# Kernel tuning notes

Hardware: AMD Instinct MI355X
Metric: run time of the kernel (lower is better)

Reference implementation:

```python
import jax, jax.numpy as jnp
import numpy as np

E, H, LQ, LC, B = 1024, 16, 1024, 512, 4
HD = E // H
FF = 4 * E
EPS = 1e-6


def _rope(x):
    # x: [B, H, L, D]; interleaved rotary embedding (lucidrains-style)
    D, L = x.shape[-1], x.shape[-2]
    inv_freq = 1.0 / (10000.0 ** (jnp.arange(0, D, 2, dtype=jnp.float32) / D))
    ang = jnp.arange(L, dtype=jnp.float32)[:, None] * inv_freq[None, :]  # [L, D/2]
    cos, sin = jnp.cos(ang), jnp.sin(ang)
    x1, x2 = x[..., 0::2], x[..., 1::2]
    r1 = x1 * cos - x2 * sin
    r2 = x1 * sin + x2 * cos
    return jnp.stack([r1, r2], axis=-1).reshape(x.shape)


def _ln(x, w, b):
    mu = jnp.mean(x, -1, keepdims=True)
    var = jnp.mean(jnp.square(x - mu), -1, keepdims=True)
    return (x - mu) * jax.lax.rsqrt(var + EPS) * w + b


def _rope_attn(x, ctx, qw, qb, kw, kb, vw, vb, pw, pb, mask):
    Bn, L, Em = x.shape
    Lc = ctx.shape[1]
    q = (x @ qw.T + qb).reshape(Bn, L, H, HD).transpose(0, 2, 1, 3)
    k = (ctx @ kw.T + kb).reshape(Bn, Lc, H, HD).transpose(0, 2, 1, 3)
    v = (ctx @ vw.T + vb).reshape(Bn, Lc, H, HD).transpose(0, 2, 1, 3)
    q, k = _rope(q), _rope(k)
    s = jnp.einsum('bhic,bhjc->bhij', q, k) / np.sqrt(HD).astype(np.float32)
    if mask is not None:
        s = jnp.where(mask[None, None], -jnp.inf, s)
    p = jax.nn.softmax(s, axis=-1)
    o = jnp.einsum('bhij,bhjc->bhic', p, v)
    o = o.transpose(0, 2, 1, 3).reshape(Bn, L, Em)
    return o @ pw.T + pb


def setup_inputs() -> dict:
    key = jax.random.key(0)
    ks = iter(jax.random.split(key, 40))
    s = 0.02
    d = {}
    d['x'] = jax.random.normal(next(ks), (B, LQ, E), jnp.float32)
    d['context'] = jax.random.normal(next(ks), (B, LC, E), jnp.float32)
    d['attn_mask'] = jnp.triu(jnp.ones((LQ, LQ), bool), k=1)  # True = masked (causal)
    for g in ('g_msa', 'g_ca', 'g_mlp'):
        d[g] = jax.random.normal(next(ks), (1, 1, E), jnp.float32) * s
    for n in ('n1', 'n2', 'n3'):
        d[n + '_w'] = jnp.ones((E,), jnp.float32)
        d[n + '_b'] = jnp.zeros((E,), jnp.float32)
    for p in ('sa', 'ca'):
        for m in ('q', 'k', 'v', 'p'):
            d[f'{p}_{m}w'] = jax.random.normal(next(ks), (E, E), jnp.float32) * s
            d[f'{p}_{m}b'] = jnp.zeros((E,), jnp.float32)
    d['fc1_w'] = jax.random.normal(next(ks), (FF, E), jnp.float32) * s
    d['fc1_b'] = jnp.zeros((FF,), jnp.float32)
    d['fc2_w'] = jax.random.normal(next(ks), (E, FF), jnp.float32) * s
    d['fc2_b'] = jnp.zeros((E,), jnp.float32)
    return d


def reference(x, context, attn_mask,
              g_msa, g_ca, g_mlp,
              n1_w, n1_b, n2_w, n2_b, n3_w, n3_b,
              sa_qw, sa_qb, sa_kw, sa_kb, sa_vw, sa_vb, sa_pw, sa_pb,
              ca_qw, ca_qb, ca_kw, ca_kb, ca_vw, ca_vb, ca_pw, ca_pb,
              fc1_w, fc1_b, fc2_w, fc2_b):
    # self-attention (causal RoPE) with zero-init learned gate
    x = x + g_msa * _rope_attn(_ln(x, n1_w, n1_b), _ln(x, n1_w, n1_b),
                               sa_qw, sa_qb, sa_kw, sa_kb, sa_vw, sa_vb,
                               sa_pw, sa_pb, attn_mask)
    # cross-attention (RoPE on both streams, no mask)
    h = _ln(x, n2_w, n2_b)
    x = x + g_ca * _rope_attn(h, context,
                              ca_qw, ca_qb, ca_kw, ca_kb, ca_vw, ca_vb,
                              ca_pw, ca_pb, None)
    # gated MLP with tanh-approx GELU
    h = _ln(x, n3_w, n3_b)
    h = jax.nn.gelu(h @ fc1_w.T + fc1_b, approximate=True) @ fc2_w.T + fc2_b
    x = x + g_mlp * h
    return x
```

## Files before the change

### kernel.cpp

```cpp
#include <hip/hip_runtime.h>
#include <math.h>

#if !__has_builtin(__builtin_amdgcn_cvt_pk_fp8_f32)
#include <hip/hip_fp8.h>
#endif

typedef __attribute__((ext_vector_type(8))) short short8;
typedef __attribute__((ext_vector_type(4))) float f32x4;
typedef __attribute__((ext_vector_type(16))) float f32x16;
typedef unsigned char u8;
typedef unsigned short u16;
typedef unsigned int u32;
typedef __attribute__((ext_vector_type(2))) u32 u32x2;
typedef __attribute__((ext_vector_type(4))) u32 u32x4;
typedef __attribute__((ext_vector_type(8))) int i32x8;
typedef unsigned long long u64;

static constexpr int E = 1024, H = 16, LQ = 1024, LC = 512, Bn = 4, FF = 4096;
static constexpr int NTOK = Bn * LQ;
static constexpr int NCTX = Bn * LC;

#define QSCALE 0.1803368801111244f
#define DEFER_THR 11.5f

static constexpr size_t OFF_TCOS   = 0;
static constexpr size_t OFF_TSIN   = OFF_TCOS + (size_t)LQ*32*4;
static constexpr size_t OFF_BSAQKV = OFF_TSIN + (size_t)LQ*32*4;
static constexpr size_t OFF_BCAKV  = OFF_BSAQKV + 16384;
static constexpr size_t OFF_WSAQKV = OFF_BCAKV + 16384;
static constexpr size_t OFF_WSAP   = OFF_WSAQKV + (size_t)3072*1024*2;
static constexpr size_t OFF_WCAQ   = OFF_WSAP   + (size_t)1024*1024*2;
static constexpr size_t OFF_WCAKV  = OFF_WCAQ   + (size_t)1024*1024*2;
static constexpr size_t OFF_WCAP   = OFF_WCAKV  + (size_t)2048*1024*2;
static constexpr size_t OFF_WFC1   = OFF_WCAP   + (size_t)1024*1024*2;
static constexpr size_t OFF_WFC2   = OFF_WFC1   + (size_t)4096*1024*2;
static constexpr size_t OFF_CTXB   = OFF_WFC2   + (size_t)1024*4096*2;
static constexpr size_t OFF_H      = OFF_CTXB   + (size_t)2048*1024*2;
static constexpr size_t OFF_QKV    = OFF_H      + (size_t)4096*1024*2;
static constexpr size_t OFF_CAQ    = OFF_QKV;
static constexpr size_t OFF_CAKV   = OFF_QKV + (size_t)4096*1024*2;
static constexpr size_t OFF_QR     = OFF_QKV + (size_t)4096*3072*2;
static constexpr size_t OFF_KR     = OFF_QR  + (size_t)4096*1024*2;
static constexpr size_t OFF_VT     = OFF_KR  + (size_t)4096*1024*2;
static constexpr size_t OFF_AO     = OFF_VT  + (size_t)4096*1024*2;
static constexpr size_t OFF_U      = OFF_QKV;
static constexpr size_t WS_NEED    = OFF_AO + (size_t)4096*1024*2;

static __device__ __forceinline__ float bf2f(u16 u) {
  union { u32 i; float f; } un; un.i = ((u32)u) << 16; return un.f;
}
static __device__ __forceinline__ u16 f2bf(float f) {
  union { float f; u32 u; } un; un.f = f;
  u32 u = un.u;
  return (u16)((u + 0x7FFFu + ((u >> 16) & 1u)) >> 16);
}
static __device__ __forceinline__ u64 pack4(u16 a, u16 b, u16 c, u16 d) {
  return (u64)a | ((u64)b << 16) | ((u64)c << 32) | ((u64)d << 48);
}
static __device__ __forceinline__ f32x4 mfma16(short8 a, short8 b, f32x4 c) {
  return __builtin_amdgcn_mfma_f32_16x16x32_bf16(a, b, c, 0, 0, 0);
}
static __device__ __forceinline__ f32x16 mfma32(short8 a, short8 b, f32x16 c) {
  return __builtin_amdgcn_mfma_f32_32x32x16_bf16(a, b, c, 0, 0, 0);
}
static __device__ __forceinline__ void gload_lds16(void* lds, const void* g) {
  __builtin_amdgcn_global_load_lds(
      (const __attribute__((address_space(1))) void*)g,
      (__attribute__((address_space(3))) void*)lds, 16, 0, 0);
}
static __device__ __forceinline__ float gelu_tanh(float x) {
  float z2 = 1.5957691216057308f * (x + 0.044715f * x * x * x);
  float e = __expf(z2);
  float r = __builtin_amdgcn_rcpf(e + 1.0f);
  return x - x * r;
}
static __device__ __forceinline__ u32 cvtpk_bf16(float lo, float hi) {
  u32 r;
  asm("v_cvt_pk_bf16_f32 %0, %1, %2" : "=v"(r) : "v"(lo), "v"(hi));
  return r;
}
static __device__ __forceinline__ u32 pack_fp8x4(float a, float b, float c, float d) {
#if __has_builtin(__builtin_amdgcn_cvt_pk_fp8_f32)
  u32 r = (u32)__builtin_amdgcn_cvt_pk_fp8_f32(a, b, 0, false);
  r = (u32)__builtin_amdgcn_cvt_pk_fp8_f32(c, d, (int)r, true);
  return r;
#else
  __hip_fp8_e4m3 qa(a), qb(b), qc(c), qd(d);
  return (u32)qa.__x | ((u32)qb.__x << 8) | ((u32)qc.__x << 16) | ((u32)qd.__x << 24);
#endif
}
static __device__ __forceinline__ u8 fp8b(float f) {
#if __has_builtin(__builtin_amdgcn_cvt_pk_fp8_f32)
  return (u8)((u32)__builtin_amdgcn_cvt_pk_fp8_f32(f, f, 0, false) & 0xFFu);
#else
  __hip_fp8_e4m3 t(f); return t.__x;
#endif
}

__global__ __launch_bounds__(256) void build_tab(float* __restrict__ ct, float* __restrict__ st) {
  int idx = blockIdx.x * 256 + threadIdx.x;
  int pos = idx >> 5, i = idx & 31;
  float inv = powf(10000.f, -(float)i * (1.f / 32.f));
  float a = (float)pos * inv;
  ct[idx] = cosf(a);
  st[idx] = sinf(a);
}

struct Cvt11 { const float* s[11]; };
__global__ __launch_bounds__(256) void cvt_all(Cvt11 a, u16* __restrict__ dst) {
  u32 gid = blockIdx.x * 256 + threadIdx.x;
  u32 s, off;
  if (gid < 2097152u)      { s = gid >> 18;                        off = gid & 262143u; }
  else if (gid < 4194304u) { return; }
  else                     { s = 10;                               off = gid - 4194304u; }
  float4 v = *(const float4*)(a.s[s] + (size_t)off * 4);
  *(u64*)(dst + (size_t)gid * 4) = pack4(f2bf(v.x), f2bf(v.y), f2bf(v.z), f2bf(v.w));
}

__global__ __launch_bounds__(256) void cvt_fp8(const float* __restrict__ s0, const float* __restrict__ s1,
                                               u8* __restrict__ d0, u8* __restrict__ d1) {
  u32 gid = blockIdx.x * 256 + threadIdx.x;
  const float* s; u8* d; u32 off;
  if (gid < 1048576u) { s = s0; d = d0; off = gid; }
  else                { s = s1; d = d1; off = gid - 1048576u; }
  float4 v = *(const float4*)(s + (size_t)off * 4);
  *(u32*)(d + (size_t)off * 4) =
      pack_fp8x4(v.x * 256.f, v.y * 256.f, v.z * 256.f, v.w * 256.f);
}

struct Cp5 { const float* s[5]; };
__global__ __launch_bounds__(256) void copy5(Cp5 a, float* __restrict__ dst) {
  int gid = blockIdx.x * 256 + threadIdx.x;
  int s = gid >> 10, off = gid & 1023;
  int doff = (s < 3) ? s * 1024 : 4096 + (s - 3) * 1024;
  dst[doff + off] = a.s[s][off];
}

__global__ __launch_bounds__(256) void ln_bf16(const float* __restrict__ x, const float* __restrict__ w,
                                               const float* __restrict__ b, u16* __restrict__ out) {
  __shared__ float red[4];
  int row = blockIdx.x, tid = threadIdx.x;
  const float* xr = x + (size_t)row * 1024;
  float4 v = ((const float4*)xr)[tid];
  float s = v.x + v.y + v.z + v.w;
#pragma unroll
  for (int off = 32; off; off >>= 1) s += __shfl_xor(s, off);
  if ((tid & 63) == 0) red[tid >> 6] = s;
  __syncthreads();
  float mean = (red[0] + red[1] + red[2] + red[3]) * (1.f / 1024.f);
  float dx = v.x - mean, dy = v.y - mean, dz = v.z - mean, dw = v.w - mean;
  float sq = dx * dx + dy * dy + dz * dz + dw * dw;
#pragma unroll
  for (int off = 32; off; off >>= 1) sq += __shfl_xor(sq, off);
  __syncthreads();
  if ((tid & 63) == 0) red[tid >> 6] = sq;
  __syncthreads();
  float var = (red[0] + red[1] + red[2] + red[3]) * (1.f / 1024.f);
  float rstd = rsqrtf(var + 1e-6f);
  float4 wv = ((const float4*)w)[tid];
  float4 bv = ((const float4*)b)[tid];
  u64 o = pack4(f2bf(dx * rstd * wv.x + bv.x), f2bf(dy * rstd * wv.y + bv.y),
                f2bf(dz * rstd * wv.z + bv.z), f2bf(dw * rstd * wv.w + bv.w));
  *(u64*)(out + (size_t)row * 1024 + tid * 4) = o;
}

__global__ __launch_bounds__(256) void ln_fp8(const float* __restrict__ x, const float* __restrict__ w,
                                              const float* __restrict__ b, u8* __restrict__ out) {
  __shared__ float red[4];
  int row = blockIdx.x, tid = threadIdx.x;
  const float* xr = x + (size_t)row * 1024;
  float4 v = ((const float4*)xr)[tid];
  float s = v.x + v.y + v.z + v.w;
#pragma unroll
  for (int off = 32; off; off >>= 1) s += __shfl_xor(s, off);
  if ((tid & 63) == 0) red[tid >> 6] = s;
  __syncthreads();
  float mean = (red[0] + red[1] + red[2] + red[3]) * (1.f / 1024.f);
  float dx = v.x - mean, dy = v.y - mean, dz = v.z - mean, dw = v.w - mean;
  float sq = dx * dx + dy * dy + dz * dz + dw * dw;
#pragma unroll
  for (int off = 32; off; off >>= 1) sq += __shfl_xor(sq, off);
  __syncthreads();
  if ((tid & 63) == 0) red[tid >> 6] = sq;
  __syncthreads();
  float var = (red[0] + red[1] + red[2] + red[3]) * (1.f / 1024.f);
  float rstd = rsqrtf(var + 1e-6f);
  float4 wv = ((const float4*)w)[tid];
  float4 bv = ((const float4*)b)[tid];
  u32 pk = pack_fp8x4((dx * rstd * wv.x + bv.x) * 16.f, (dy * rstd * wv.y + bv.y) * 16.f,
                      (dz * rstd * wv.z + bv.z) * 16.f, (dw * rstd * wv.w + bv.w) * 16.f);
  *(u32*)(out + (size_t)row * 1024 + tid * 4) = pk;
}

struct RopeJob { const u16* src; u16* dst; int ld, col0, Lper, T, mode; float scale; };
struct Rope3 { RopeJob j[3]; };
__global__ __launch_bounds__(128) void rope3(Rope3 a, const float* __restrict__ cosT,
                                             const float* __restrict__ sinT) {
  RopeJob jb = a.j[blockIdx.y];
  int t = blockIdx.x;
  if (t >= jb.T) return;
  int b = t / jb.Lper, l = t - b * jb.Lper;
  int tid = threadIdx.x;
  int e0 = tid * 8;
  int h = e0 >> 6, d0 = e0 & 63;
  short8 vv = *(const short8*)(jb.src + (size_t)t * jb.ld + jb.col0 + e0);
  if (jb.mode == 0) {
    short8 ov;
#pragma unroll
    for (int j = 0; j < 4; ++j) {
      float x1 = bf2f((u16)vv[2 * j]);
      float x2 = bf2f((u16)vv[2 * j + 1]);
      int i = (d0 >> 1) + j;
      float c = cosT[l * 32 + i], s = sinT[l * 32 + i];
      ov[2 * j]     = (short)f2bf((x1 * c - x2 * s) * jb.scale);
      ov[2 * j + 1] = (short)f2bf((x1 * s + x2 * c) * jb.scale);
    }
    *(short8*)(jb.dst + (((size_t)b * H + h) * jb.Lper + l) * 64 + d0) = ov;
  } else {
#pragma unroll
    for (int m = 0; m < 8; ++m)
      jb.dst[(((size_t)b * H + h) * 64 + d0 + m) * jb.Lper + l] = (u16)vv[m];
  }
}

enum { EPI_BF16 = 0, EPI_GELU = 1, EPI_RESID = 2 };

template <int EPI>
__global__ __launch_bounds__(512, 4) void gemm2(const u16* __restrict__ A, const u16* __restrict__ W,
                                                const float* __restrict__ bias, u16* outb, float* outf,
                                                const float* res, const float* __restrict__ gate,
                                                int M, int N, int K) {
  __shared__ u16 As[2][128 * 64];
  __shared__ u16 Bs[2][128 * 64];

  int nwg = gridDim.x * gridDim.y;
  int bid = blockIdx.y * gridDim.x + blockIdx.x;
  int cpx = nwg >> 3;
  int swz = (bid & 7) * cpx + (bid >> 3);
  int bx = swz % gridDim.x;
  int by = swz / gridDim.x;
  int row0 = by * 128, col0 = bx * 128;

  int tid = threadIdx.x;
  int lane = tid & 63, wid = tid >> 6;
  int wr = wid >> 2, wc = wid & 3;
  int lr = lane & 15, lg = lane >> 4;

  size_t a_off0, a_off1, b_off0, b_off1;
  int l_off0 = tid * 8, l_off1 = (512 + tid) * 8;
  {
    int q = tid, r = q >> 3, p = q & 7, sp = p ^ (r & 7);
    a_off0 = (size_t)(row0 + r) * K + sp * 8;
    b_off0 = (size_t)(col0 + r) * K + sp * 8;
    q = 512 + tid; r = q >> 3; p = q & 7; sp = p ^ (r & 7);
    a_off1 = (size_t)(row0 + r) * K + sp * 8;
    b_off1 = (size_t)(col0 + r) * K + sp * 8;
  }

  f32x4 acc[4][2] = {};

  const int nkt = K >> 6;
  {
    gload_lds16(&As[0][l_off0], A + a_off0);
    gload_lds16(&Bs[0][l_off0], W + b_off0);
    gload_lds16(&As[0][l_off1], A + a_off1);
    gload_lds16(&Bs[0][l_off1], W + b_off1);
  }
  __syncthreads();

  for (int kt = 0; kt < nkt; ++kt) {
    int cur = kt & 1;
    if (kt + 1 < nkt) {
      int k0 = (kt + 1) << 6;
      gload_lds16(&As[cur ^ 1][l_off0], A + a_off0 + k0);
      gload_lds16(&Bs[cur ^ 1][l_off0], W + b_off0 + k0);
      gload_lds16(&As[cur ^ 1][l_off1], A + a_off1 + k0);
      gload_lds16(&Bs[cur ^ 1][l_off1], W + b_off1 + k0);
    }
#pragma unroll
    for (int kk = 0; kk < 2; ++kk) {
      short8 af[4], bfr[2];
#pragma unroll
      for (int m = 0; m < 4; ++m) {
        int r = wr * 64 + m * 16 + lr;
        int sc = (kk * 4 + lg) ^ (r & 7);
        af[m] = *(const short8*)(&As[cur][r * 64 + sc * 8]);
      }
#pragma unroll
      for (int n = 0; n < 2; ++n) {
        int r = wc * 32 + n * 16 + lr;
        int sc = (kk * 4 + lg) ^ (r & 7);
        bfr[n] = *(const short8*)(&Bs[cur][r * 64 + sc * 8]);
      }
#pragma unroll
      for (int m = 0; m < 4; ++m)
#pragma unroll
        for (int n = 0; n < 2; ++n)
          acc[m][n] = mfma16(af[m], bfr[n], acc[m][n]);
    }
    __syncthreads();
  }

  if (EPI == EPI_BF16 || EPI == EPI_GELU) {
    u16* Ct = &As[0][0];
#pragma unroll
    for (int n = 0; n < 2; ++n) {
      int c = wc * 32 + n * 16 + lr;
      float bv = bias[col0 + c];
#pragma unroll
      for (int m = 0; m < 4; ++m) {
#pragma unroll
        for (int i = 0; i < 4; ++i) {
          int r = wr * 64 + m * 16 + lg * 4 + i;
          float v = acc[m][n][i] + bv;
          Ct[r * 128 + c] = f2bf(EPI == EPI_GELU ? gelu_tanh(v) : v);
        }
      }
    }
    __syncthreads();
#pragma unroll
    for (int j = 0; j < 4; ++j) {
      u32 q = (u32)tid + j * 512;
      u32 r = q >> 4, ck = q & 15;
      short8 v = *(const short8*)(Ct + r * 128 + ck * 8);
      *(short8*)(outb + (size_t)(row0 + r) * N + col0 + ck * 8) = v;
    }
  } else {
#pragma unroll
    for (int n = 0; n < 2; ++n) {
      int cg = col0 + wc * 32 + n * 16 + lr;
      float bv = bias[cg];
#pragma unroll
      for (int m = 0; m < 4; ++m) {
#pragma unroll
        for (int i = 0; i < 4; ++i) {
          int rg = row0 + wr * 64 + m * 16 + lg * 4 + i;
          float v = acc[m][n][i] + bv;
          float r = res[(size_t)rg * N + cg];
          outf[(size_t)rg * N + cg] = r + gate[cg] * v;
        }
      }
    }
  }
}

enum { E8_GELU = 0, E8_RESID = 1 };

template <int EPI>
__global__ __launch_bounds__(256, 2) void gemm8(const u8* __restrict__ A, const u8* __restrict__ W,
                                                const float* __restrict__ bias, u8* outb, float* outf,
                                                const float* res, const float* __restrict__ gate,
                                                int M, int N, int K) {
  __shared__ u8 As[2][128 * 128];
  __shared__ u8 Bs[2][128 * 128];

  int nwg = gridDim.x * gridDim.y;
  int bid = blockIdx.y * gridDim.x + blockIdx.x;
  int cpx = nwg >> 3;
  int swz = (bid & 7) * cpx + (bid >> 3);
  int bx = swz % gridDim.x, by = swz / gridDim.x;
  int row0 = by * 128, col0 = bx * 128;

  int tid = threadIdx.x;
  int lane = tid & 63, wid = tid >> 6;
  int wr = wid >> 1, wc = wid & 1;
  int lr = lane & 15, lg = lane >> 4;

  u32 aoff[4], boff[4];
  int ldso[4];
#pragma unroll
  for (int j = 0; j < 4; ++j) {
    int q = tid + j * 256;
    int r = q >> 3, p = q & 7, sp = p ^ (r & 7);
    aoff[j] = (u32)(row0 + r) * (u32)K + sp * 16;
    boff[j] = (u32)(col0 + r) * (u32)K + sp * 16;
    ldso[j] = q * 16;
  }

  f32x4 acc[4][4] = {};
  const int nkt = K >> 7;

  auto rdfrag = [&](const u8* base, int r, i32x8& f) {
    const u8* rp = base + r * 128;
    int ck = lg * 2;
    u32x4 lo = *(const u32x4*)(rp + ((ck) ^ (r & 7)) * 16);
    u32x4 hh = *(const u32x4*)(rp + ((ck + 1) ^ (r & 7)) * 16);
    i32x8 v;
    v[0] = (int)lo[0]; v[1] = (int)lo[1]; v[2] = (int)lo[2]; v[3] = (int)lo[3];
    v[4] = (int)hh[0]; v[5] = (int)hh[1]; v[6] = (int)hh[2]; v[7] = (int)hh[3];
    f = v;
  };

#pragma unroll
  for (int j = 0; j < 4; ++j) {
    gload_lds16(&As[0][ldso[j]], A + aoff[j]);
    gload_lds16(&Bs[0][ldso[j]], W + boff[j]);
  }
  __syncthreads();

  for (int kt = 0; kt < nkt; ++kt) {
    int cur = kt & 1;
    if (kt + 1 < nkt) {
      int k0 = (kt + 1) << 7;
#pragma unroll
      for (int j = 0; j < 4; ++j) {
        gload_lds16(&As[cur ^ 1][ldso[j]], A + aoff[j] + k0);
        gload_lds16(&Bs[cur ^ 1][ldso[j]], W + boff[j] + k0);
      }
    }
    i32x8 a[4], b[4];
#pragma unroll
    for (int m = 0; m < 4; ++m) rdfrag(&As[cur][0], wr * 64 + m * 16 + lr, a[m]);
#pragma unroll
    for (int n = 0; n < 4; ++n) rdfrag(&Bs[cur][0], wc * 64 + n * 16 + lr, b[n]);
    __builtin_amdgcn_s_setprio(1);
#pragma unroll
    for (int m = 0; m < 4; ++m)
#pragma unroll
      for (int n = 0; n < 4; ++n)
        acc[m][n] = __builtin_amdgcn_mfma_scale_f32_16x16x128_f8f6f4(
            a[m], b[n], acc[m][n], 0, 0, 0, 0x7F7F7F7F, 0, 0x7F7F7F7F);
    __builtin_amdgcn_s_setprio(0);
    __syncthreads();
  }

  constexpr float SCL = 1.f / 4096.f;
  if (EPI == E8_GELU) {
    u8* Ct = &As[0][0];
#pragma unroll
    for (int n = 0; n < 4; ++n) {
      int cl = wc * 64 + n * 16 + lr;
      float bv = bias[col0 + cl];
#pragma unroll
      for (int m = 0; m < 4; ++m) {
#pragma unroll
        for (int i = 0; i < 4; ++i) {
          int rl = wr * 64 + m * 16 + lg * 4 + i;
          float v = acc[m][n][i] * SCL + bv;
          Ct[rl * 128 + cl] = fp8b(gelu_tanh(v) * 16.f);
        }
      }
    }
    __syncthreads();
#pragma unroll
    for (int j = 0; j < 4; ++j) {
      int q = tid + j * 256;
      int r = q >> 3, ck = q & 7;
      *(u32x4*)(outb + (size_t)(row0 + r) * N + col0 + ck * 16) =
          *(const u32x4*)(Ct + r * 128 + ck * 16);
    }
  } else {
#pragma unroll
    for (int n = 0; n < 4; ++n) {
      int cg = col0 + wc * 64 + n * 16 + lr;
      float bv = bias[cg], gv = gate[cg];
#pragma unroll
      for (int m = 0; m < 4; ++m) {
#pragma unroll
        for (int i = 0; i < 4; ++i) {
          int rg = row0 + wr * 64 + m * 16 + lg * 4 + i;
          float v = acc[m][n][i] * SCL + bv;
          float r = res[(size_t)rg * N + cg];
          outf[(size_t)rg * N + cg] = r + gv * v;
        }
      }
    }
  }
}

template <int MASKED, int PRE>
static __device__ __forceinline__ void attn_tile3(short8* kf, const u16* KtNext,
                                                  const u16* Vp0, const u16* Vp1,
                                                  const short8* qf, int kb, int q0, int l31, int hi,
                                                  float& m, float& lsum, f32x16& o0, f32x16& o1) {
  short8 vf0[4], vf1[4];
#pragma unroll
  for (int ks = 0; ks < 4; ++ks) {
    vf0[ks] = *(const short8*)(Vp0 + ks * 16 + hi * 8);
    vf1[ks] = *(const short8*)(Vp1 + ks * 16 + hi * 8);
  }
  f32x16 s0 = {}, s1 = {};
  __builtin_amdgcn_s_setprio(1);
#pragma unroll
  for (int s = 0; s < 4; ++s) {
    s0 = mfma32(kf[s], qf[s], s0);
    s1 = mfma32(kf[4 + s], qf[s], s1);
  }
  __builtin_amdgcn_s_setprio(0);
  if (PRE) {
    const u16* kp0 = KtNext + (size_t)l31 * 64 + hi * 8;
    const u16* kp1 = KtNext + (size_t)(32 + l31) * 64 + hi * 8;
#pragma unroll
    for (int s = 0; s < 4; ++s) {
      kf[s] = *(const short8*)(kp0 + s * 16);
      kf[4 + s] = *(const short8*)(kp1 + s * 16);
    }
  }
  if (MASKED) {
    int qg = q0 + l31;
#pragma unroll
    for (int r = 0; r < 16; ++r) {
      int kk = kb + (r & 3) + 8 * (r >> 2) + 4 * hi;
      if (kk > qg) s0[r] = -INFINITY;
      if (kk + 32 > qg) s1[r] = -INFINITY;
    }
  }
  float pm = -INFINITY;
#pragma unroll
  for (int r = 0; r < 16; ++r) pm = fmaxf(pm, fmaxf(s0[r], s1[r]));
  pm = fmaxf(pm, __shfl_xor(pm, 32));
  if (!__all(pm <= m + DEFER_THR)) {
    float mn = fmaxf(m, pm);
    float al = exp2f(m - mn);
    m = mn;
    lsum *= al;
#pragma unroll
    for (int r = 0; r < 16; ++r) {
      float alr = __shfl(al, (r & 3) + 8 * (r >> 2) + 4 * hi);
      o0[r] *= alr;
      o1[r] *= alr;
    }
  }
  float ts = 0.f;
#pragma unroll
  for (int r = 0; r < 16; ++r) {
    float p0 = exp2f(s0[r] - m);
    float p1 = exp2f(s1[r] - m);
    s0[r] = p0; s1[r] = p1;
    ts += p0 + p1;
  }
  ts += __shfl_xor(ts, 32);
  lsum += ts;
  auto pack8 = [&](float a0, float a1, float a2, float a3,
                   float a4, float a5, float a6, float a7) -> short8 {
    u32 c0 = cvtpk_bf16(a0, a1), c1 = cvtpk_bf16(a2, a3);
    u32 c2 = cvtpk_bf16(a4, a5), c3 = cvtpk_bf16(a6, a7);
    u32x2 r02 = __builtin_amdgcn_permlane32_swap(c0, c2, false, false);
    u32x2 r13 = __builtin_amdgcn_permlane32_swap(c1, c3, false, false);
    u32x4 w;
    w[0] = r02[0]; w[1] = r13[0]; w[2] = r02[1]; w[3] = r13[1];
    return __builtin_bit_cast(short8, w);
  };
  short8 pa0 = pack8(s0[0], s0[1], s0[2], s0[3], s0[4], s0[5], s0[6], s0[7]);
  short8 pa1 = pack8(s0[8], s0[9], s0[10], s0[11], s0[12], s0[13], s0[14], s0[15]);
  short8 pa2 = pack8(s1[0], s1[1], s1[2], s1[3], s1[4], s1[5], s1[6], s1[7]);
  short8 pa3 = pack8(s1[8], s1[9], s1[10], s1[11], s1[12], s1[13], s1[14], s1[15]);
  short8 pa[4] = {pa0, pa1, pa2, pa3};
  __builtin_amdgcn_s_setprio(1);
#pragma unroll
  for (int ks = 0; ks < 4; ++ks) {
    o0 = mfma32(pa[ks], vf0[ks], o0);
    o1 = mfma32(pa[ks], vf1[ks], o1);
  }
  __builtin_amdgcn_s_setprio(0);
}

template <int CAUSAL>
__global__ __launch_bounds__(256) void flash_attn2(const u16* __restrict__ Q, const u16* __restrict__ K,
                                                   const u16* __restrict__ Vt, u16* __restrict__ O,
                                                   int Lq, int Lk) {
  const int wid = threadIdx.x >> 6, lane = threadIdx.x & 63;
  const int l31 = lane & 31, hi = lane >> 5;
  int wg = blockIdx.x * 4 + wid;
  int bh = wg & 63;
  int qc = wg >> 6;
  if (CAUSAL) qc = (Lq >> 5) - 1 - qc;
  int q0 = qc << 5;

  const u16* Qb = Q + ((size_t)bh * Lq + q0) * 64;
  const u16* Kb = K + (size_t)bh * Lk * 64;
  const u16* Vb = Vt + (size_t)bh * 64 * Lk;

  short8 qf[4];
#pragma unroll
  for (int s = 0; s < 4; ++s) qf[s] = *(const short8*)(Qb + (size_t)l31 * 64 + s * 16 + hi * 8);

  f32x16 o0 = {}, o1 = {};
  float m = -INFINITY, lsum = 0.f;

  const u16* Kt = Kb;
  const u16* Vp0 = Vb + (size_t)l31 * Lk;
  const u16* Vp1 = Vb + (size_t)(32 + l31) * Lk;

  short8 kf[8];
  {
    const u16* kp0 = Kt + (size_t)l31 * 64 + hi * 8;
    const u16* kp1 = Kt + (size_t)(32 + l31) * 64 + hi * 8;
#pragma unroll
    for (int s = 0; s < 4; ++s) {
      kf[s] = *(const short8*)(kp0 + s * 16);
      kf[4 + s] = *(const short8*)(kp1 + s * 16);
    }
  }

  int nt = CAUSAL ? ((q0 >> 6) + 1) : (Lk >> 6);
  for (int t = 0; t < nt - 1; ++t) {
    attn_tile3<0, 1>(kf, Kt + 64 * 64, Vp0, Vp1, qf, t * 64, q0, l31, hi, m, lsum, o0, o1);
    Kt += 64 * 64; Vp0 += 64; Vp1 += 64;
  }
  if (CAUSAL)
    attn_tile3<1, 0>(kf, nullptr, Vp0, Vp1, qf, (nt - 1) * 64, q0, l31, hi, m, lsum, o0, o1);
  else
    attn_tile3<0, 0>(kf, nullptr, Vp0, Vp1, qf, (nt - 1) * 64, q0, l31, hi, m, lsum, o0, o1);

  float myinv = 1.f / lsum;
  int b = bh >> 4, h = bh & 15;
#pragma unroll
  for (int r = 0; r < 16; ++r) {
    int cr = (r & 3) + 8 * (r >> 2) + 4 * hi;
    float li = __shfl(myinv, cr);
    u16* op = O + ((size_t)b * Lq + q0 + cr) * 1024 + h * 64;
    op[l31] = f2bf(o0[r] * li);
    op[32 + l31] = f2bf(o1[r] * li);
  }
}

extern "C" void kernel_launch(void* const* d_in, const int* in_sizes, int n_in,
                              void* d_out, int out_size, void* d_ws, size_t ws_size,
                              hipStream_t stream) {
  (void)in_sizes; (void)n_in; (void)out_size;
  if (ws_size < WS_NEED) return;

  const float* x     = (const float*)d_in[0];
  const float* ctx   = (const float*)d_in[1];
  const float* g_msa = (const float*)d_in[3];
  const float* g_ca  = (const float*)d_in[4];
  const float* g_mlp = (const float*)d_in[5];
  const float* n1w = (const float*)d_in[6],  *n1b = (const float*)d_in[7];
  const float* n2w = (const float*)d_in[8],  *n2b = (const float*)d_in[9];
  const float* n3w = (const float*)d_in[10], *n3b = (const float*)d_in[11];
  const float* sa_qw = (const float*)d_in[12], *sa_kw = (const float*)d_in[14];
  const float* sa_vw = (const float*)d_in[16], *sa_pw = (const float*)d_in[18];
  const float* sa_qb = (const float*)d_in[13], *sa_kb = (const float*)d_in[15];
  const float* sa_vb = (const float*)d_in[17], *sa_pb = (const float*)d_in[19];
  const float* ca_qw = (const float*)d_in[20], *ca_qb = (const float*)d_in[21];
  const float* ca_kw = (const float*)d_in[22], *ca_kb = (const float*)d_in[23];
  const float* ca_vw = (const float*)d_in[24], *ca_vb = (const float*)d_in[25];
  const float* ca_pw = (const float*)d_in[26], *ca_pb = (const float*)d_in[27];
  const float* fc1w = (const float*)d_in[28], *fc1b = (const float*)d_in[29];
  const float* fc2w = (const float*)d_in[30], *fc2b = (const float*)d_in[31];

  char* ws = (char*)d_ws;
  float* out = (float*)d_out;
  float* tcos = (float*)(ws + OFF_TCOS);
  float* tsin = (float*)(ws + OFF_TSIN);
  u16* Hb   = (u16*)(ws + OFF_H);
  u16* QKV  = (u16*)(ws + OFF_QKV);
  u16* QR   = (u16*)(ws + OFF_QR);
  u16* KR   = (u16*)(ws + OFF_KR);
  u16* VT   = (u16*)(ws + OFF_VT);
  u16* AO   = (u16*)(ws + OFF_AO);
  u8*  H8   = (u8*)(ws + OFF_H);
  u8*  U8   = (u8*)(ws + OFF_U);
  u8*  W8FC1 = (u8*)(ws + OFF_QR);
  u8*  W8FC2 = (u8*)(ws + OFF_KR);

  build_tab<<<dim3(128), dim3(256), 0, stream>>>(tcos, tsin);

  Cvt11 ca;
  ca.s[0] = sa_qw; ca.s[1] = sa_kw; ca.s[2] = sa_vw; ca.s[3] = sa_pw;
  ca.s[4] = ca_qw; ca.s[5] = ca_kw; ca.s[6] = ca_vw; ca.s[7] = ca_pw;
  ca.s[8] = fc1w;  ca.s[9] = fc2w;  ca.s[10] = ctx;
  cvt_all<<<dim3(18432), dim3(256), 0, stream>>>(ca, (u16*)(ws + OFF_WSAQKV));
  Cp5 cp;
  cp.s[0] = sa_qb; cp.s[1] = sa_kb; cp.s[2] = sa_vb; cp.s[3] = ca_kb; cp.s[4] = ca_vb;
  copy5<<<dim3(20), dim3(256), 0, stream>>>(cp, (float*)(ws + OFF_BSAQKV));

  ln_bf16<<<dim3(NTOK), dim3(256), 0, stream>>>(x, n1w, n1b, Hb);
  gemm2<EPI_BF16><<<dim3(3072 / 128, NTOK / 128), dim3(512), 0, stream>>>(
      Hb, (u16*)(ws + OFF_WSAQKV), (float*)(ws + OFF_BSAQKV), QKV, nullptr, nullptr, nullptr,
      NTOK, 3072, 1024);
  {
    Rope3 r;
    r.j[0] = {QKV, QR, 3072, 0,    LQ, NTOK, 0, QSCALE};
    r.j[1] = {QKV, KR, 3072, 1024, LQ, NTOK, 0, 1.0f};
    r.j[2] = {QKV, VT, 3072, 2048, LQ, NTOK, 1, 1.0f};
    rope3<<<dim3(NTOK, 3), dim3(128), 0, stream>>>(r, tcos, tsin);
  }
  flash_attn2<1><<<dim3(512), dim3(256), 0, stream>>>(QR, KR, VT, AO, LQ, LQ);
  gemm2<EPI_RESID><<<dim3(1024 / 128, NTOK / 128), dim3(512), 0, stream>>>(
      AO, (u16*)(ws + OFF_WSAP), sa_pb, nullptr, out, x, g_msa, NTOK, 1024, 1024);

  ln_bf16<<<dim3(NTOK), dim3(256), 0, stream>>>(out, n2w, n2b, Hb);
  gemm2<EPI_BF16><<<dim3(1024 / 128, NTOK / 128), dim3(512), 0, stream>>>(
      Hb, (u16*)(ws + OFF_WCAQ), ca_qb, (u16*)(ws + OFF_CAQ), nullptr, nullptr, nullptr,
      NTOK, 1024, 1024);
  gemm2<EPI_BF16><<<dim3(2048 / 128, NCTX / 128), dim3(512), 0, stream>>>(
      (u16*)(ws + OFF_CTXB), (u16*)(ws + OFF_WCAKV), (float*)(ws + OFF_BCAKV),
      (u16*)(ws + OFF_CAKV), nullptr, nullptr, nullptr, NCTX, 2048, 1024);
  {
    Rope3 r;
    r.j[0] = {(u16*)(ws + OFF_CAQ),  QR, 1024, 0,    LQ, NTOK, 0, QSCALE};
    r.j[1] = {(u16*)(ws + OFF_CAKV), KR, 2048, 0,    LC, NCTX, 0, 1.0f};
    r.j[2] = {(u16*)(ws + OFF_CAKV), VT, 2048, 1024, LC, NCTX, 1, 1.0f};
    rope3<<<dim3(NTOK, 3), dim3(128), 0, stream>>>(r, tcos, tsin);
  }
  flash_attn2<0><<<dim3(512), dim3(256), 0, stream>>>(QR, KR, VT, AO, LQ, LC);
  gemm2<EPI_RESID><<<dim3(1024 / 128, NTOK / 128), dim3(512), 0, stream>>>(
      AO, (u16*)(ws + OFF_WCAP), ca_pb, nullptr, out, out, g_ca, NTOK, 1024, 1024);

  cvt_fp8<<<dim3(8192), dim3(256), 0, stream>>>(fc1w, fc2w, W8FC1, W8FC2);
  ln_fp8<<<dim3(NTOK), dim3(256), 0, stream>>>(out, n3w, n3b, H8);
  gemm8<E8_GELU><<<dim3(4096 / 128, NTOK / 128), dim3(256), 0, stream>>>(
      H8, W8FC1, fc1b, U8, nullptr, nullptr, nullptr, NTOK, 4096, 1024);
  gemm8<E8_RESID><<<dim3(1024 / 128, NTOK / 128), dim3(256), 0, stream>>>(
      U8, W8FC2, fc2b, nullptr, out, out, g_mlp, NTOK, 1024, 4096);
}
```

Baseline: 380.1 us.

## Run self-attn QKV projection in FP8 and split-K the FC2 GEMM with atomics

Replaces the bf16 LN+QKV GEMM for self-attention with an FP8 LayerNorm and an FP8 GEMM that has a new bf16-output epilogue, quantizing sa_q/k/v weights alongside the FC1/FC2 weights in one merged conversion kernel. FC2 is split along K into two chunks that accumulate into the output with atomicAdd, after a small kernel pre-adds the gated bias. The aim is to halve the operand bytes for the QKV GEMM and to double the block count for the small-N FC2 GEMM to fill the GPU. The trade-offs are lower precision on Q/K/V, atomic traffic with non-deterministic summation order, and an extra pass over the output.

Measured after the change: 369.2 us. -2.9%, faster.

```diff
diff --git a/kernel.cpp b/kernel.cpp
--- a/kernel.cpp
+++ b/kernel.cpp
@@ -46,6 +46,10 @@
 static constexpr size_t OFF_U      = OFF_QKV;
 static constexpr size_t WS_NEED    = OFF_AO + (size_t)4096*1024*2;
 
+static constexpr size_t OFF_W8QKV = OFF_WFC1;
+static constexpr size_t OFF_W8FC1 = OFF_W8QKV + (size_t)3072*1024;
+static constexpr size_t OFF_W8FC2 = OFF_W8FC1 + (size_t)4096*1024;
+
 static __device__ __forceinline__ float bf2f(u16 u) {
   union { u32 i; float f; } un; un.i = ((u32)u) << 16; return un.f;
 }
@@ -110,19 +114,24 @@
 __global__ __launch_bounds__(256) void cvt_all(Cvt11 a, u16* __restrict__ dst) {
   u32 gid = blockIdx.x * 256 + threadIdx.x;
   u32 s, off;
-  if (gid < 2097152u)      { s = gid >> 18;                        off = gid & 262143u; }
+  if (gid < 2097152u)      { s = gid >> 18; if (s < 3) return;     off = gid & 262143u; }
   else if (gid < 4194304u) { return; }
   else                     { s = 10;                               off = gid - 4194304u; }
   float4 v = *(const float4*)(a.s[s] + (size_t)off * 4);
   *(u64*)(dst + (size_t)gid * 4) = pack4(f2bf(v.x), f2bf(v.y), f2bf(v.z), f2bf(v.w));
 }
 
-__global__ __launch_bounds__(256) void cvt_fp8(const float* __restrict__ s0, const float* __restrict__ s1,
-                                               u8* __restrict__ d0, u8* __restrict__ d1) {
+__global__ __launch_bounds__(256) void cvt_fp8b(const float* __restrict__ qw, const float* __restrict__ kw,
+                                                const float* __restrict__ vw, const float* __restrict__ f1,
+                                                const float* __restrict__ f2,
+                                                u8* __restrict__ d_qkv, u8* __restrict__ d_f1,
+                                                u8* __restrict__ d_f2) {
   u32 gid = blockIdx.x * 256 + threadIdx.x;
-  const float* s; u8* d; u32 off;
-  if (gid < 1048576u) { s = s0; d = d0; off = gid; }
-  else                { s = s1; d = d1; off = gid - 1048576u; }
+  u32 seg = gid >> 18, off = gid & 262143u;
+  const float* s; u8* d;
+  if (seg < 3)      { s = seg == 0 ? qw : (seg == 1 ? kw : vw); d = d_qkv + (size_t)seg * 1048576; }
+  else if (seg < 7) { s = f1 + (size_t)(seg - 3) * 1048576;     d = d_f1  + (size_t)(seg - 3) * 1048576; }
+  else              { s = f2 + (size_t)(seg - 7) * 1048576;     d = d_f2  + (size_t)(seg - 7) * 1048576; }
   float4 v = *(const float4*)(s + (size_t)off * 4);
   *(u32*)(d + (size_t)off * 4) =
       pack_fp8x4(v.x * 256.f, v.y * 256.f, v.z * 256.f, v.w * 256.f);
@@ -134,6 +143,18 @@
   int s = gid >> 10, off = gid & 1023;
   int doff = (s < 3) ? s * 1024 : 4096 + (s - 3) * 1024;
   dst[doff + off] = a.s[s][off];
+}
+
+__global__ __launch_bounds__(256) void init_bias_gate(float* __restrict__ out, const float* __restrict__ bias,
+                                                      const float* __restrict__ gate) {
+  int i = (blockIdx.x * 256 + threadIdx.x) * 4;
+  int c = i & 1023;
+  float4 o = *(float4*)(out + i);
+  o.x += gate[c] * bias[c];
+  o.y += gate[c + 1] * bias[c + 1];
+  o.z += gate[c + 2] * bias[c + 2];
+  o.w += gate[c + 3] * bias[c + 3];
+  *(float4*)(out + i) = o;
 }
 
 __global__ __launch_bounds__(256) void ln_bf16(const float* __restrict__ x, const float* __restrict__ w,
@@ -344,13 +365,13 @@
   }
 }
 
-enum { E8_GELU = 0, E8_RESID = 1 };
+enum { E8_BF16 = 0, E8_GELU = 1, E8_ATOMIC = 2 };
 
 template <int EPI>
 __global__ __launch_bounds__(256, 2) void gemm8(const u8* __restrict__ A, const u8* __restrict__ W,
-                                                const float* __restrict__ bias, u8* outb, float* outf,
-                                                const float* res, const float* __restrict__ gate,
-                                                int M, int N, int K) {
+                                                const float* __restrict__ bias, u16* outb16,
+                                                u8* outb8, float* outf, const float* __restrict__ gate,
+                                                int M, int N, int K, int kchunks) {
   __shared__ u8 As[2][128 * 128];
   __shared__ u8 Bs[2][128 * 128];
 
@@ -361,6 +382,9 @@
   int bx = swz % gridDim.x, by = swz / gridDim.x;
   int row0 = by * 128, col0 = bx * 128;
 
+  const int Kc = K / kchunks;
+  const int kbase = blockIdx.z * Kc;
+
   int tid = threadIdx.x;
   int lane = tid & 63, wid = tid >> 6;
   int wr = wid >> 1, wc = wid & 1;
@@ -378,7 +402,7 @@
   }
 
   f32x4 acc[4][4] = {};
-  const int nkt = K >> 7;
+  const int nkt = Kc >> 7;
 
   auto rdfrag = [&](const u8* base, int r, i32x8& f) {
     const u8* rp = base + r * 128;
@@ -393,15 +417,15 @@
 
 #pragma unroll
   for (int j = 0; j < 4; ++j) {
-    gload_lds16(&As[0][ldso[j]], A + aoff[j]);
-    gload_lds16(&Bs[0][ldso[j]], W + boff[j]);
+    gload_lds16(&As[0][ldso[j]], A + aoff[j] + kbase);
+    gload_lds16(&Bs[0][ldso[j]], W + boff[j] + kbase);
   }
   __syncthreads();
 
   for (int kt = 0; kt < nkt; ++kt) {
     int cur = kt & 1;
     if (kt + 1 < nkt) {
-      int k0 = (kt + 1) << 7;
+      int k0 = kbase + ((kt + 1) << 7);
 #pragma unroll
       for (int j = 0; j < 4; ++j) {
         gload_lds16(&As[cur ^ 1][ldso[j]], A + aoff[j] + k0);
@@ -425,7 +449,30 @@
   }
 
   constexpr float SCL = 1.f / 4096.f;
-  if (EPI == E8_GELU) {
+  if (EPI == E8_BF16) {
+    u16* Ct = (u16*)&As[0][0];
+#pragma unroll
+    for (int n = 0; n < 4; ++n) {
+      int cl = wc * 64 + n * 16 + lr;
+      float bv = bias[col0 + cl];
+#pragma unroll
+      for (int m = 0; m < 4; ++m) {
+#pragma unroll
+        for (int i = 0; i < 4; ++i) {
+          int rl = wr * 64 + m * 16 + lg * 4 + i;
+          Ct[rl * 128 + cl] = f2bf(acc[m][n][i] * SCL + bv);
+        }
+      }
+    }
+    __syncthreads();
+#pragma unroll
+    for (int j = 0; j < 8; ++j) {
+      u32 q = (u32)tid + j * 256;
+      u32 r = q >> 4, ck = q & 15;
+      short8 v = *(const short8*)(Ct + r * 128 + ck * 8);
+      *(short8*)(outb16 + (size_t)(row0 + r) * N + col0 + ck * 8) = v;
+    }
+  } else if (EPI == E8_GELU) {
     u8* Ct = &As[0][0];
 #pragma unroll
     for (int n = 0; n < 4; ++n) {
@@ -446,22 +493,20 @@
     for (int j = 0; j < 4; ++j) {
       int q = tid + j * 256;
       int r = q >> 3, ck = q & 7;
-      *(u32x4*)(outb + (size_t)(row0 + r) * N + col0 + ck * 16) =
+      *(u32x4*)(outb8 + (size_t)(row0 + r) * N + col0 + ck * 16) =
           *(const u32x4*)(Ct + r * 128 + ck * 16);
     }
   } else {
 #pragma unroll
     for (int n = 0; n < 4; ++n) {
       int cg = col0 + wc * 64 + n * 16 + lr;
-      float bv = bias[cg], gv = gate[cg];
+      float gv = gate[cg];
 #pragma unroll
       for (int m = 0; m < 4; ++m) {
 #pragma unroll
         for (int i = 0; i < 4; ++i) {
           int rg = row0 + wr * 64 + m * 16 + lg * 4 + i;
-          float v = acc[m][n][i] * SCL + bv;
-          float r = res[(size_t)rg * N + cg];
-          outf[(size_t)rg * N + cg] = r + gv * v;
+          atomicAdd(&outf[(size_t)rg * N + cg], gv * (acc[m][n][i] * SCL));
         }
       }
     }
@@ -652,8 +697,9 @@
   u16* AO   = (u16*)(ws + OFF_AO);
   u8*  H8   = (u8*)(ws + OFF_H);
   u8*  U8   = (u8*)(ws + OFF_U);
-  u8*  W8FC1 = (u8*)(ws + OFF_QR);
-  u8*  W8FC2 = (u8*)(ws + OFF_KR);
+  u8*  W8QKV = (u8*)(ws + OFF_W8QKV);
+  u8*  W8FC1 = (u8*)(ws + OFF_W8FC1);
+  u8*  W8FC2 = (u8*)(ws + OFF_W8FC2);
 
   build_tab<<<dim3(128), dim3(256), 0, stream>>>(tcos, tsin);
 
@@ -662,14 +708,16 @@
   ca.s[4] = ca_qw; ca.s[5] = ca_kw; ca.s[6] = ca_vw; ca.s[7] = ca_pw;
   ca.s[8] = fc1w;  ca.s[9] = fc2w;  ca.s[10] = ctx;
   cvt_all<<<dim3(18432), dim3(256), 0, stream>>>(ca, (u16*)(ws + OFF_WSAQKV));
+  cvt_fp8b<<<dim3(11264), dim3(256), 0, stream>>>(sa_qw, sa_kw, sa_vw, fc1w, fc2w,
+                                                  W8QKV, W8FC1, W8FC2);
   Cp5 cp;
   cp.s[0] = sa_qb; cp.s[1] = sa_kb; cp.s[2] = sa_vb; cp.s[3] = ca_kb; cp.s[4] = ca_vb;
   copy5<<<dim3(20), dim3(256), 0, stream>>>(cp, (float*)(ws + OFF_BSAQKV));
 
-  ln_bf16<<<dim3(NTOK), dim3(256), 0, stream>>>(x, n1w, n1b, Hb);
-  gemm2<EPI_BF16><<<dim3(3072 / 128, NTOK / 128), dim3(512), 0, stream>>>(
-      Hb, (u16*)(ws + OFF_WSAQKV), (float*)(ws + OFF_BSAQKV), QKV, nullptr, nullptr, nullptr,
-      NTOK, 3072, 1024);
+  ln_fp8<<<dim3(NTOK), dim3(256), 0, stream>>>(x, n1w, n1b, H8);
+  gemm8<E8_BF16><<<dim3(3072 / 128, NTOK / 128), dim3(256), 0, stream>>>(
+      H8, W8QKV, (float*)(ws + OFF_BSAQKV), QKV, nullptr, nullptr, nullptr,
+      NTOK, 3072, 1024, 1);
   {
     Rope3 r;
     r.j[0] = {QKV, QR, 3072, 0,    LQ, NTOK, 0, QSCALE};
@@ -699,10 +747,10 @@
   gemm2<EPI_RESID><<<dim3(1024 / 128, NTOK / 128), dim3(512), 0, stream>>>(
       AO, (u16*)(ws + OFF_WCAP), ca_pb, nullptr, out, out, g_ca, NTOK, 1024, 1024);
 
-  cvt_fp8<<<dim3(8192), dim3(256), 0, stream>>>(fc1w, fc2w, W8FC1, W8FC2);
   ln_fp8<<<dim3(NTOK), dim3(256), 0, stream>>>(out, n3w, n3b, H8);
   gemm8<E8_GELU><<<dim3(4096 / 128, NTOK / 128), dim3(256), 0, stream>>>(
-      H8, W8FC1, fc1b, U8, nullptr, nullptr, nullptr, NTOK, 4096, 1024);
-  gemm8<E8_RESID><<<dim3(1024 / 128, NTOK / 128), dim3(256), 0, stream>>>(
-      U8, W8FC2, fc2b, nullptr, out, out, g_mlp, NTOK, 1024, 4096);
-}
+      H8, W8FC1, fc1b, nullptr, U8, nullptr, nullptr, NTOK, 4096, 1024, 1);
+  init_bias_gate<<<dim3(4096), dim3(256), 0, stream>>>(out, fc2b, g_mlp);
+  gemm8<E8_ATOMIC><<<dim3(1024 / 128, NTOK / 128, 2), dim3(256), 0, stream>>>(
+      U8, W8FC2, nullptr, nullptr, nullptr, out, g_mlp, NTOK, 1024, 4096, 2);
+}
```
